# Performance work log

Measured on AMD Instinct MI355X. Metric: run time of the kernel, lower is better.

Reference implementation:

```python
import jax, jax.numpy as jnp
import numpy as np


def _hat(v):
    # v: (...,3) -> (...,3,3) skew-symmetric
    x, y, z = v[..., 0], v[..., 1], v[..., 2]
    O = jnp.zeros_like(x)
    return jnp.stack([
        jnp.stack([O, -z, y], axis=-1),
        jnp.stack([z, O, -x], axis=-1),
        jnp.stack([-y, x, O], axis=-1),
    ], axis=-2)


def _exp_so3(omega):
    # Rodrigues: (...,3) axis-angle -> (...,3,3)
    theta = jnp.maximum(jnp.linalg.norm(omega, axis=-1, keepdims=True), 1e-12)
    k = omega / theta
    K = _hat(k)
    I = jnp.broadcast_to(jnp.eye(3, dtype=omega.dtype), omega.shape[:-1] + (3, 3))
    s = jnp.sin(theta)[..., None]
    c = jnp.cos(theta)[..., None]
    R = I + s * K + (1.0 - c) * (K @ K)
    small = (theta[..., 0] < 1e-4)[..., None, None]
    return jnp.where(small, I + _hat(omega), R)


def setup_inputs() -> dict:
    key = jax.random.key(0)
    ks = jax.random.split(key, 10)
    N, M, H = 262144, 64, 64
    X0 = jax.random.normal(ks[0], (N, 3), jnp.float32)
    G0 = jax.random.normal(ks[1], (M, 3), jnp.float32)
    W = jax.random.uniform(ks[2], (N, M), jnp.float32)
    so3_vec = jax.random.normal(ks[3], (M, 3), jnp.float32) * 0.5
    trans = jax.random.normal(ks[4], (M, 3), jnp.float32) * 0.1
    wproj_w = jax.random.normal(ks[5], (16, M), jnp.float32) * 0.1
    wproj_b = jnp.zeros((16,), jnp.float32)
    w1 = jax.random.normal(ks[6], (H, 19), jnp.float32) * 0.1
    b1 = jnp.zeros((H,), jnp.float32)
    w2 = jax.random.normal(ks[7], (H, H), jnp.float32) * 0.1
    b2 = jnp.zeros((H,), jnp.float32)
    w3 = jax.random.normal(ks[8], (3, H), jnp.float32) * 0.1
    b3 = jnp.zeros((3,), jnp.float32)
    return {"X0": X0, "G0": G0, "W": W, "so3_vec": so3_vec, "trans": trans,
            "wproj_w": wproj_w, "wproj_b": wproj_b,
            "w1": w1, "b1": b1, "w2": w2, "b2": b2, "w3": w3, "b3": b3}


def reference(X0, G0, W, so3_vec, trans, wproj_w, wproj_b, w1, b1, w2, b2, w3, b3):
    # normalized skinning weights (mask is all-ones; row sums > 0 with rand fill)
    Wn = W / (jnp.sum(W, axis=1, keepdims=True) + 1e-12)  # (N,M)
    R = _exp_so3(so3_vec)                                  # (M,3,3)
    d = X0[:, None, :] - G0[None, :, :]                    # (N,M,3)
    Rp = jnp.einsum('mkj,nmj->nmk', R, d)                  # (N,M,3)
    q = Rp + G0[None, :, :] + trans[None, :, :]            # (N,M,3)
    skinned = jnp.einsum('nm,nmk->nk', Wn, q)              # (N,3)
    # residual branch
    Rb = jnp.einsum('nm,mkj->nkj', Wn, R)                  # (N,3,3) blended rotation
    tb = Wn @ trans                                        # (N,3)
    local = jnp.einsum('nji,nj->ni', Rb, skinned - tb)     # Rb^T @ (s - tb)
    wfeat = Wn @ wproj_w.T + wproj_b                       # (N,16)
    h = jnp.concatenate([local, wfeat], axis=1)            # (N,19)
    h = jax.nn.relu(h @ w1.T + b1)
    h = jax.nn.relu(h @ w2.T + b2)
    delta_local = h @ w3.T + b3                            # (N,3)
    delta_world = jnp.einsum('nij,nj->ni', Rb, delta_local)
    return skinned + delta_world
```

## Files before the change

kernel.cpp:

```cpp
#include <hip/hip_runtime.h>
#include <math.h>

typedef float f32x4 __attribute__((ext_vector_type(4)));
typedef _Float16 f16x8 __attribute__((ext_vector_type(8)));
typedef unsigned int u32;
typedef unsigned int u32x2 __attribute__((ext_vector_type(2)));
typedef unsigned int u32x4 __attribute__((ext_vector_type(4)));

#define MJ 64
#define HID 64
#define STR 144
#define TP 32
#define REGSZ (TP*STR)
#define SLICE (2*REGSZ)

static __device__ __forceinline__ u32 pkhf(float a, float b) {
  unsigned short ua = __builtin_bit_cast(unsigned short, (_Float16)a);
  unsigned short ub = __builtin_bit_cast(unsigned short, (_Float16)b);
  return (u32)ua | ((u32)ub << 16);
}

static __device__ __forceinline__ f32x4 mfma16(f16x8 a, f16x8 b, f32x4 c) {
  return __builtin_amdgcn_mfma_f32_16x16x32_f16(a, b, c, 0, 0, 0);
}

__global__ void rig_prep(const float* __restrict__ G0, const float* __restrict__ so3,
                         const float* __restrict__ trans, const float* __restrict__ wproj_w,
                         const float* __restrict__ wproj_b,
                         const float* __restrict__ w1, const float* __restrict__ b1,
                         const float* __restrict__ w2,
                         _Float16* __restrict__ FT1, _Float16* __restrict__ FT2,
                         _Float16* __restrict__ FT3) {
  const int t = threadIdx.x;
  {
    const float ox = so3[3*t+0], oy = so3[3*t+1], oz = so3[3*t+2];
    const float th = sqrtf(ox*ox + oy*oy + oz*oz);
    float R[9];
    if (th < 1e-4f) {
      R[0]=1.f;  R[1]=-oz; R[2]=oy;
      R[3]=oz;   R[4]=1.f; R[5]=-ox;
      R[6]=-oy;  R[7]=ox;  R[8]=1.f;
    } else {
      const float it = 1.f/th;
      const float kx=ox*it, ky=oy*it, kz=oz*it;
      const float s=sinf(th), c=cosf(th), mc=1.f-c;
      R[0]=c+kx*kx*mc;     R[1]=kx*ky*mc-kz*s;  R[2]=kx*kz*mc+ky*s;
      R[3]=ky*kx*mc+kz*s;  R[4]=c+ky*ky*mc;     R[5]=ky*kz*mc-kx*s;
      R[6]=kz*kx*mc-ky*s;  R[7]=kz*ky*mc+kx*s;  R[8]=c+kz*kz*mc;
    }
    const float gx=G0[3*t], gy=G0[3*t+1], gz=G0[3*t+2];
    const float tx=trans[3*t], ty=trans[3*t+1], tz=trans[3*t+2];
    float feat[32];
    #pragma unroll
    for (int i=0;i<9;i++) feat[i]=R[i];
    feat[9]  = gx + tx - (R[0]*gx + R[1]*gy + R[2]*gz);
    feat[10] = gy + ty - (R[3]*gx + R[4]*gy + R[5]*gz);
    feat[11] = gz + tz - (R[6]*gx + R[7]*gy + R[8]*gz);
    feat[12]=tx; feat[13]=ty; feat[14]=tz;
    feat[15]=1.0f;
    #pragma unroll
    for (int i=0;i<16;i++) feat[16+i] = wproj_w[i*MJ + t];
    #pragma unroll
    for (int f=0;f<32;f++) FT1[f*64 + t] = (_Float16)feat[f];
  }
  {
    float fold = b1[t];
    #pragma unroll
    for (int j=0;j<16;j++) fold = fmaf(w1[t*19 + 3 + j], wproj_b[j], fold);
    #pragma unroll
    for (int k=0;k<19;k++) FT2[t*32+k] = (_Float16)w1[t*19+k];
    FT2[t*32+19] = (_Float16)fold;
    #pragma unroll
    for (int k=20;k<32;k++) FT2[t*32+k] = (_Float16)0.0f;
  }
  for (int k=0;k<64;k++) FT3[t*64+k] = (_Float16)w2[t*64+k];
}

__global__ __launch_bounds__(256, 4)
void rig_main(const float* __restrict__ X0, const float* __restrict__ W,
              const _Float16* __restrict__ FT1, const _Float16* __restrict__ FT2,
              const _Float16* __restrict__ FT3,
              const float* __restrict__ b2, const float* __restrict__ w3,
              const float* __restrict__ b3,
              float* __restrict__ out, int Ntot) {
  __shared__ __align__(16) unsigned char smem[4*SLICE];
  const int tid  = threadIdx.x;
  const int wid  = tid >> 6;
  const int lane = tid & 63;
  const int lo   = lane & 15;
  const int hi   = lane >> 4;
  const int pl   = lane & 31;
  const int P0   = blockIdx.x * (4*TP) + wid * TP;
  unsigned char* Areg = smem + wid * SLICE;
  unsigned char* Breg = Areg + REGSZ;

  const float x0 = X0[(size_t)(P0+pl)*3+0];
  const float x1 = X0[(size_t)(P0+pl)*3+1];
  const float x2 = X0[(size_t)(P0+pl)*3+2];

  {
    f32x4 q[8];
    const f32x4* Wq = (const f32x4*)(W + (size_t)P0 * MJ);
    #pragma unroll
    for (int i=0;i<8;i++) q[i] = Wq[i*64 + lane];
    #pragma unroll
    for (int i=0;i<8;i++) {
      const int fidx = i*64 + lane;
      const int row = fidx >> 4, c4 = fidx & 15;
      u32x2 p; p.x = pkhf(q[i][0], q[i][1]); p.y = pkhf(q[i][2], q[i][3]);
      *(u32x2*)(Areg + row*STR + c4*8) = p;
    }
  }
  __syncthreads();

  {
    f16x8 a1[2][2];
    #pragma unroll
    for (int ft=0; ft<2; ft++)
      #pragma unroll
      for (int ks=0; ks<2; ks++)
        a1[ft][ks] = *(const f16x8*)(FT1 + (ft*16+lo)*64 + ks*32 + hi*8);
    f32x4 acc[2][2];
    const f32x4 z = {0.f,0.f,0.f,0.f};
    #pragma unroll
    for (int ft=0; ft<2; ft++)
      #pragma unroll
      for (int pt=0; pt<2; pt++) acc[ft][pt] = z;
    #pragma unroll
    for (int pt=0; pt<2; pt++) {
      #pragma unroll
      for (int ks=0; ks<2; ks++) {
        f16x8 bfrag = *(const f16x8*)(Areg + (pt*16+lo)*STR + ks*64 + hi*16);
        acc[0][pt] = mfma16(a1[0][ks], bfrag, acc[0][pt]);
        acc[1][pt] = mfma16(a1[1][ks], bfrag, acc[1][pt]);
      }
    }
    #pragma unroll
    for (int pt=0; pt<2; pt++)
      #pragma unroll
      for (int ft=0; ft<2; ft++)
        *(f32x4*)(Breg + (pt*16+lo)*STR + ft*64 + hi*16) = acc[ft][pt];
  }
  __syncthreads();

  float Rb[9], sk0, sk1, sk2;
  {
    float v[32];
    #pragma unroll
    for (int i=0;i<8;i++) {
      f32x4 t4 = *(const f32x4*)(Breg + pl*STR + i*16);
      v[4*i+0]=t4[0]; v[4*i+1]=t4[1]; v[4*i+2]=t4[2]; v[4*i+3]=t4[3];
    }
    const float inv = 1.0f/(v[15] + 1e-12f);
    #pragma unroll
    for (int i=0;i<9;i++) Rb[i]=v[i]*inv;
    const float cb0=v[9]*inv,  cb1=v[10]*inv, cb2=v[11]*inv;
    const float tb0=v[12]*inv, tb1=v[13]*inv, tb2=v[14]*inv;
    sk0 = fmaf(Rb[0],x0, fmaf(Rb[1],x1, fmaf(Rb[2],x2, cb0)));
    sk1 = fmaf(Rb[3],x0, fmaf(Rb[4],x1, fmaf(Rb[5],x2, cb1)));
    sk2 = fmaf(Rb[6],x0, fmaf(Rb[7],x1, fmaf(Rb[8],x2, cb2)));
    const float u0=sk0-tb0, u1=sk1-tb1, u2=sk2-tb2;
    const float l0 = Rb[0]*u0 + Rb[3]*u1 + Rb[6]*u2;
    const float l1 = Rb[1]*u0 + Rb[4]*u1 + Rb[7]*u2;
    const float l2 = Rb[2]*u0 + Rb[5]*u1 + Rb[8]*u2;
    float wf[16];
    #pragma unroll
    for (int j=0;j<16;j++) wf[j] = v[16+j]*inv;
    u32x4 h0, h1v, h2v, h3;
    h0.x = pkhf(l0, l1);       h0.y = pkhf(l2, wf[0]);
    h0.z = pkhf(wf[1], wf[2]); h0.w = pkhf(wf[3], wf[4]);
    h1v.x = pkhf(wf[5], wf[6]);  h1v.y = pkhf(wf[7], wf[8]);
    h1v.z = pkhf(wf[9], wf[10]); h1v.w = pkhf(wf[11], wf[12]);
    h2v.x = pkhf(wf[13], wf[14]); h2v.y = pkhf(wf[15], 1.0f);
    h2v.z = 0u; h2v.w = 0u;
    h3.x = 0u; h3.y = 0u; h3.z = 0u; h3.w = 0u;
    *(u32x4*)(Areg + pl*STR +  0) = h0;
    *(u32x4*)(Areg + pl*STR + 16) = h1v;
    *(u32x4*)(Areg + pl*STR + 32) = h2v;
    *(u32x4*)(Areg + pl*STR + 48) = h3;
  }
  __syncthreads();

  {
    f16x8 bh[2];
    #pragma unroll
    for (int pt=0; pt<2; pt++)
      bh[pt] = *(const f16x8*)(Areg + (pt*16+lo)*STR + hi*16);
    #pragma unroll
    for (int nh=0; nh<2; nh++) {
      f16x8 a2[2];
      #pragma unroll
      for (int n2=0; n2<2; n2++)
        a2[n2] = *(const f16x8*)(FT2 + ((nh*2+n2)*16+lo)*32 + hi*8);
      f32x4 c2[2][2];
      const f32x4 z = {0.f,0.f,0.f,0.f};
      #pragma unroll
      for (int n2=0;n2<2;n2++)
        #pragma unroll
        for (int pt=0;pt<2;pt++) c2[n2][pt] = z;
      #pragma unroll
      for (int pt=0; pt<2; pt++)
        #pragma unroll
        for (int n2=0; n2<2; n2++)
          c2[n2][pt] = mfma16(a2[n2], bh[pt], c2[n2][pt]);
      #pragma unroll
      for (int n2=0; n2<2; n2++)
        #pragma unroll
        for (int pt=0; pt<2; pt++) {
          f32x4 r = c2[n2][pt];
          u32x2 wv;
          wv.x = pkhf(fmaxf(r[0],0.f), fmaxf(r[1],0.f));
          wv.y = pkhf(fmaxf(r[2],0.f), fmaxf(r[3],0.f));
          *(u32x2*)(Breg + (pt*16+lo)*STR + (nh*2+n2)*32 + hi*8) = wv;
        }
    }
  }
  __syncthreads();

  {
    f16x8 bh1[2][2];
    #pragma unroll
    for (int pt=0; pt<2; pt++)
      #pragma unroll
      for (int ks=0; ks<2; ks++)
        bh1[pt][ks] = *(const f16x8*)(Breg + (pt*16+lo)*STR + ks*64 + hi*16);
    #pragma unroll
    for (int nh=0; nh<2; nh++) {
      f16x8 a3[2][2];
      #pragma unroll
      for (int n2=0; n2<2; n2++)
        #pragma unroll
        for (int ks=0; ks<2; ks++)
          a3[n2][ks] = *(const f16x8*)(FT3 + ((nh*2+n2)*16+lo)*64 + ks*32 + hi*8);
      f32x4 c3[2][2];
      const f32x4 z = {0.f,0.f,0.f,0.f};
      #pragma unroll
      for (int n2=0;n2<2;n2++)
        #pragma unroll
        for (int pt=0;pt<2;pt++) c3[n2][pt] = z;
      #pragma unroll
      for (int pt=0; pt<2; pt++)
        #pragma unroll
        for (int ks=0; ks<2; ks++)
          #pragma unroll
          for (int n2=0; n2<2; n2++)
            c3[n2][pt] = mfma16(a3[n2][ks], bh1[pt][ks], c3[n2][pt]);
      #pragma unroll
      for (int n2=0; n2<2; n2++) {
        const f32x4 vb2 = *(const f32x4*)(b2 + (nh*2+n2)*16 + hi*4);
        #pragma unroll
        for (int pt=0; pt<2; pt++) {
          f32x4 r = c3[n2][pt];
          u32x2 wv;
          wv.x = pkhf(fmaxf(r[0]+vb2[0],0.f), fmaxf(r[1]+vb2[1],0.f));
          wv.y = pkhf(fmaxf(r[2]+vb2[2],0.f), fmaxf(r[3]+vb2[3],0.f));
          *(u32x2*)(Areg + (pt*16+lo)*STR + (nh*2+n2)*32 + hi*8) = wv;
        }
      }
    }
  }
  __syncthreads();

  {
    float d0 = b3[0], d1 = b3[1], d2 = b3[2];
    #pragma unroll
    for (int i8=0; i8<8; i8++) {
      f16x8 hv = *(const f16x8*)(Areg + pl*STR + i8*16);
      #pragma unroll
      for (int e=0; e<8; e++) {
        const float a = (float)hv[e];
        const int j = i8*8 + e;
        d0 = fmaf(a, w3[      j], d0);
        d1 = fmaf(a, w3[ 64 + j], d1);
        d2 = fmaf(a, w3[128 + j], d2);
      }
    }
    if (lane < TP) {
      const float dw0 = Rb[0]*d0 + Rb[1]*d1 + Rb[2]*d2;
      const float dw1 = Rb[3]*d0 + Rb[4]*d1 + Rb[5]*d2;
      const float dw2 = Rb[6]*d0 + Rb[7]*d1 + Rb[8]*d2;
      const size_t o = (size_t)(P0+pl)*3;
      out[o+0] = sk0 + dw0;
      out[o+1] = sk1 + dw1;
      out[o+2] = sk2 + dw2;
    }
  }
}

extern "C" void kernel_launch(void* const* d_in, const int* in_sizes, int n_in,
                              void* d_out, int out_size, void* d_ws, size_t ws_size,
                              hipStream_t stream) {
  const float* X0      = (const float*)d_in[0];
  const float* G0      = (const float*)d_in[1];
  const float* W       = (const float*)d_in[2];
  const float* so3     = (const float*)d_in[3];
  const float* trans   = (const float*)d_in[4];
  const float* wproj_w = (const float*)d_in[5];
  const float* wproj_b = (const float*)d_in[6];
  const float* w1      = (const float*)d_in[7];
  const float* b1      = (const float*)d_in[8];
  const float* w2      = (const float*)d_in[9];
  const float* b2      = (const float*)d_in[10];
  const float* w3      = (const float*)d_in[11];
  const float* b3      = (const float*)d_in[12];
  float* out = (float*)d_out;

  const int Ntot = in_sizes[0] / 3;

  _Float16* FT1 = (_Float16*)d_ws;
  _Float16* FT2 = (_Float16*)((char*)d_ws + 4096);
  _Float16* FT3 = (_Float16*)((char*)d_ws + 8192);

  rig_prep<<<1, 64, 0, stream>>>(G0, so3, trans, wproj_w, wproj_b,
                                 w1, b1, w2, FT1, FT2, FT3);
  rig_main<<<Ntot/(4*TP), 256, 0, stream>>>(X0, W, FT1, FT2, FT3,
                                            b2, w3, b3, out, Ntot);
}
```

Baseline: 33.72 us.

## Loop four tiles per block with register prefetch of next W tile

Each block now processes four 128-point tiles in a loop, prefetching the next tile's W and X0 into registers while the current tile runs its MFMA phases. Block-wide syncs become a lighter custom barrier that only waits on LDS counters, so outstanding global prefetches are not drained at each phase. The prep kernel is widened to 256 threads so the w2 conversion is split across more threads. In exchange the grid shrinks fourfold and register pressure rises from holding two W tiles, which may reduce occupancy or parallelism on a 256-CU device.

Result: slower. 54.49 us (+61.6%).

```diff
diff --git a/kernel.cpp b/kernel.cpp
--- a/kernel.cpp
+++ b/kernel.cpp
@@ -13,6 +13,8 @@
 #define TP 32
 #define REGSZ (TP*STR)
 #define SLICE (2*REGSZ)
+#define TILES 4
+#define BPTS 128
 
 static __device__ __forceinline__ u32 pkhf(float a, float b) {
   unsigned short ua = __builtin_bit_cast(unsigned short, (_Float16)a);
@@ -22,6 +24,13 @@
 
 static __device__ __forceinline__ f32x4 mfma16(f16x8 a, f16x8 b, f32x4 c) {
   return __builtin_amdgcn_mfma_f32_16x16x32_f16(a, b, c, 0, 0, 0);
+}
+
+static __device__ __forceinline__ void phase_sync() {
+  asm volatile("s_waitcnt lgkmcnt(0)" ::: "memory");
+  __builtin_amdgcn_sched_barrier(0);
+  __builtin_amdgcn_s_barrier();
+  __builtin_amdgcn_sched_barrier(0);
 }
 
 __global__ void rig_prep(const float* __restrict__ G0, const float* __restrict__ so3,
@@ -32,7 +41,7 @@
                          _Float16* __restrict__ FT1, _Float16* __restrict__ FT2,
                          _Float16* __restrict__ FT3) {
   const int t = threadIdx.x;
-  {
+  if (t < MJ) {
     const float ox = so3[3*t+0], oy = so3[3*t+1], oz = so3[3*t+2];
     const float th = sqrtf(ox*ox + oy*oy + oz*oz);
     float R[9];
@@ -62,18 +71,21 @@
     for (int i=0;i<16;i++) feat[16+i] = wproj_w[i*MJ + t];
     #pragma unroll
     for (int f=0;f<32;f++) FT1[f*64 + t] = (_Float16)feat[f];
+
+    float fold = b1[t];
+    #pragma unroll
+    for (int j=0;j<16;j++) fold = fmaf(w1[t*19 + 3 + j], wproj_b[j], fold);
+    #pragma unroll
+    for (int k=0;k<19;k++) FT2[t*32+k] = (_Float16)w1[t*19+k];
+    FT2[t*32+19] = (_Float16)fold;
+    #pragma unroll
+    for (int k=20;k<32;k++) FT2[t*32+k] = (_Float16)0.0f;
   }
   {
-    float fold = b1[t];
-    #pragma unroll
-    for (int j=0;j<16;j++) fold = fmaf(w1[t*19 + 3 + j], wproj_b[j], fold);
-    #pragma unroll
-    for (int k=0;k<19;k++) FT2[t*32+k] = (_Float16)w1[t*19+k];
-    FT2[t*32+19] = (_Float16)fold;
-    #pragma unroll
-    for (int k=20;k<32;k++) FT2[t*32+k] = (_Float16)0.0f;
+    const int row = t >> 2, cb = (t & 3) * 16;
+    #pragma unroll
+    for (int k=0;k<16;k++) FT3[row*64 + cb + k] = (_Float16)w2[row*64 + cb + k];
   }
-  for (int k=0;k<64;k++) FT3[t*64+k] = (_Float16)w2[t*64+k];
 }
 
 __global__ __launch_bounds__(256, 4)
@@ -90,200 +102,222 @@
   const int lo   = lane & 15;
   const int hi   = lane >> 4;
   const int pl   = lane & 31;
-  const int P0   = blockIdx.x * (4*TP) + wid * TP;
+  const int base = blockIdx.x * (TILES*BPTS);
   unsigned char* Areg = smem + wid * SLICE;
   unsigned char* Breg = Areg + REGSZ;
 
-  const float x0 = X0[(size_t)(P0+pl)*3+0];
-  const float x1 = X0[(size_t)(P0+pl)*3+1];
-  const float x2 = X0[(size_t)(P0+pl)*3+2];
-
+  f32x4 qc[8];
   {
-    f32x4 q[8];
-    const f32x4* Wq = (const f32x4*)(W + (size_t)P0 * MJ);
-    #pragma unroll
-    for (int i=0;i<8;i++) q[i] = Wq[i*64 + lane];
+    const f32x4* Wq = (const f32x4*)(W + (size_t)(base + wid*TP) * MJ);
+    #pragma unroll
+    for (int i=0;i<8;i++) qc[i] = Wq[i*64 + lane];
+  }
+  float xc0 = X0[(size_t)(base + wid*TP + pl)*3+0];
+  float xc1 = X0[(size_t)(base + wid*TP + pl)*3+1];
+  float xc2 = X0[(size_t)(base + wid*TP + pl)*3+2];
+
+  #pragma unroll
+  for (int t=0; t<TILES; ++t) {
+    const int P0 = base + t*BPTS + wid*TP;
+
     #pragma unroll
     for (int i=0;i<8;i++) {
       const int fidx = i*64 + lane;
       const int row = fidx >> 4, c4 = fidx & 15;
-      u32x2 p; p.x = pkhf(q[i][0], q[i][1]); p.y = pkhf(q[i][2], q[i][3]);
+      u32x2 p; p.x = pkhf(qc[i][0], qc[i][1]); p.y = pkhf(qc[i][2], qc[i][3]);
       *(u32x2*)(Areg + row*STR + c4*8) = p;
     }
-  }
-  __syncthreads();
-
-  {
-    f16x8 a1[2][2];
-    #pragma unroll
-    for (int ft=0; ft<2; ft++)
-      #pragma unroll
-      for (int ks=0; ks<2; ks++)
-        a1[ft][ks] = *(const f16x8*)(FT1 + (ft*16+lo)*64 + ks*32 + hi*8);
-    f32x4 acc[2][2];
-    const f32x4 z = {0.f,0.f,0.f,0.f};
-    #pragma unroll
-    for (int ft=0; ft<2; ft++)
-      #pragma unroll
-      for (int pt=0; pt<2; pt++) acc[ft][pt] = z;
-    #pragma unroll
-    for (int pt=0; pt<2; pt++) {
-      #pragma unroll
-      for (int ks=0; ks<2; ks++) {
-        f16x8 bfrag = *(const f16x8*)(Areg + (pt*16+lo)*STR + ks*64 + hi*16);
-        acc[0][pt] = mfma16(a1[0][ks], bfrag, acc[0][pt]);
-        acc[1][pt] = mfma16(a1[1][ks], bfrag, acc[1][pt]);
-      }
-    }
-    #pragma unroll
-    for (int pt=0; pt<2; pt++)
+    f32x4 qn[8];
+    float xn0=0.f, xn1=0.f, xn2=0.f;
+    if (t+1 < TILES) {
+      const f32x4* Wqn = (const f32x4*)(W + (size_t)(P0 + BPTS) * MJ);
+      #pragma unroll
+      for (int i=0;i<8;i++) qn[i] = Wqn[i*64 + lane];
+      xn0 = X0[(size_t)(P0 + BPTS + pl)*3+0];
+      xn1 = X0[(size_t)(P0 + BPTS + pl)*3+1];
+      xn2 = X0[(size_t)(P0 + BPTS + pl)*3+2];
+    }
+    phase_sync();
+
+    {
+      f16x8 a1[2][2];
       #pragma unroll
       for (int ft=0; ft<2; ft++)
-        *(f32x4*)(Breg + (pt*16+lo)*STR + ft*64 + hi*16) = acc[ft][pt];
-  }
-  __syncthreads();
-
-  float Rb[9], sk0, sk1, sk2;
-  {
-    float v[32];
-    #pragma unroll
-    for (int i=0;i<8;i++) {
-      f32x4 t4 = *(const f32x4*)(Breg + pl*STR + i*16);
-      v[4*i+0]=t4[0]; v[4*i+1]=t4[1]; v[4*i+2]=t4[2]; v[4*i+3]=t4[3];
-    }
-    const float inv = 1.0f/(v[15] + 1e-12f);
-    #pragma unroll
-    for (int i=0;i<9;i++) Rb[i]=v[i]*inv;
-    const float cb0=v[9]*inv,  cb1=v[10]*inv, cb2=v[11]*inv;
-    const float tb0=v[12]*inv, tb1=v[13]*inv, tb2=v[14]*inv;
-    sk0 = fmaf(Rb[0],x0, fmaf(Rb[1],x1, fmaf(Rb[2],x2, cb0)));
-    sk1 = fmaf(Rb[3],x0, fmaf(Rb[4],x1, fmaf(Rb[5],x2, cb1)));
-    sk2 = fmaf(Rb[6],x0, fmaf(Rb[7],x1, fmaf(Rb[8],x2, cb2)));
-    const float u0=sk0-tb0, u1=sk1-tb1, u2=sk2-tb2;
-    const float l0 = Rb[0]*u0 + Rb[3]*u1 + Rb[6]*u2;
-    const float l1 = Rb[1]*u0 + Rb[4]*u1 + Rb[7]*u2;
-    const float l2 = Rb[2]*u0 + Rb[5]*u1 + Rb[8]*u2;
-    float wf[16];
-    #pragma unroll
-    for (int j=0;j<16;j++) wf[j] = v[16+j]*inv;
-    u32x4 h0, h1v, h2v, h3;
-    h0.x = pkhf(l0, l1);       h0.y = pkhf(l2, wf[0]);
-    h0.z = pkhf(wf[1], wf[2]); h0.w = pkhf(wf[3], wf[4]);
-    h1v.x = pkhf(wf[5], wf[6]);  h1v.y = pkhf(wf[7], wf[8]);
-    h1v.z = pkhf(wf[9], wf[10]); h1v.w = pkhf(wf[11], wf[12]);
-    h2v.x = pkhf(wf[13], wf[14]); h2v.y = pkhf(wf[15], 1.0f);
-    h2v.z = 0u; h2v.w = 0u;
-    h3.x = 0u; h3.y = 0u; h3.z = 0u; h3.w = 0u;
-    *(u32x4*)(Areg + pl*STR +  0) = h0;
-    *(u32x4*)(Areg + pl*STR + 16) = h1v;
-    *(u32x4*)(Areg + pl*STR + 32) = h2v;
-    *(u32x4*)(Areg + pl*STR + 48) = h3;
-  }
-  __syncthreads();
-
-  {
-    f16x8 bh[2];
-    #pragma unroll
-    for (int pt=0; pt<2; pt++)
-      bh[pt] = *(const f16x8*)(Areg + (pt*16+lo)*STR + hi*16);
-    #pragma unroll
-    for (int nh=0; nh<2; nh++) {
-      f16x8 a2[2];
-      #pragma unroll
-      for (int n2=0; n2<2; n2++)
-        a2[n2] = *(const f16x8*)(FT2 + ((nh*2+n2)*16+lo)*32 + hi*8);
-      f32x4 c2[2][2];
+        #pragma unroll
+        for (int ks=0; ks<2; ks++)
+          a1[ft][ks] = *(const f16x8*)(FT1 + (ft*16+lo)*64 + ks*32 + hi*8);
+      f32x4 acc[2][2];
       const f32x4 z = {0.f,0.f,0.f,0.f};
       #pragma unroll
-      for (int n2=0;n2<2;n2++)
-        #pragma unroll
-        for (int pt=0;pt<2;pt++) c2[n2][pt] = z;
+      for (int ft=0; ft<2; ft++)
+        #pragma unroll
+        for (int pt=0; pt<2; pt++) acc[ft][pt] = z;
+      #pragma unroll
+      for (int pt=0; pt<2; pt++) {
+        #pragma unroll
+        for (int ks=0; ks<2; ks++) {
+          f16x8 bfrag = *(const f16x8*)(Areg + (pt*16+lo)*STR + ks*64 + hi*16);
+          acc[0][pt] = mfma16(a1[0][ks], bfrag, acc[0][pt]);
+          acc[1][pt] = mfma16(a1[1][ks], bfrag, acc[1][pt]);
+        }
+      }
       #pragma unroll
       for (int pt=0; pt<2; pt++)
         #pragma unroll
+        for (int ft=0; ft<2; ft++)
+          *(f32x4*)(Breg + (pt*16+lo)*STR + ft*64 + hi*16) = acc[ft][pt];
+    }
+    phase_sync();
+
+    float Rb[9], sk0, sk1, sk2;
+    {
+      float v[32];
+      #pragma unroll
+      for (int i=0;i<8;i++) {
+        f32x4 t4 = *(const f32x4*)(Breg + pl*STR + i*16);
+        v[4*i+0]=t4[0]; v[4*i+1]=t4[1]; v[4*i+2]=t4[2]; v[4*i+3]=t4[3];
+      }
+      const float inv = 1.0f/(v[15] + 1e-12f);
+      #pragma unroll
+      for (int i=0;i<9;i++) Rb[i]=v[i]*inv;
+      const float cb0=v[9]*inv,  cb1=v[10]*inv, cb2=v[11]*inv;
+      const float tb0=v[12]*inv, tb1=v[13]*inv, tb2=v[14]*inv;
+      sk0 = fmaf(Rb[0],xc0, fmaf(Rb[1],xc1, fmaf(Rb[2],xc2, cb0)));
+      sk1 = fmaf(Rb[3],xc0, fmaf(Rb[4],xc1, fmaf(Rb[5],xc2, cb1)));
+      sk2 = fmaf(Rb[6],xc0, fmaf(Rb[7],xc1, fmaf(Rb[8],xc2, cb2)));
+      const float u0=sk0-tb0, u1=sk1-tb1, u2=sk2-tb2;
+      const float l0 = Rb[0]*u0 + Rb[3]*u1 + Rb[6]*u2;
+      const float l1 = Rb[1]*u0 + Rb[4]*u1 + Rb[7]*u2;
+      const float l2 = Rb[2]*u0 + Rb[5]*u1 + Rb[8]*u2;
+      float wf[16];
+      #pragma unroll
+      for (int j=0;j<16;j++) wf[j] = v[16+j]*inv;
+      u32x4 h0, h1v, h2v, h3;
+      h0.x = pkhf(l0, l1);       h0.y = pkhf(l2, wf[0]);
+      h0.z = pkhf(wf[1], wf[2]); h0.w = pkhf(wf[3], wf[4]);
+      h1v.x = pkhf(wf[5], wf[6]);  h1v.y = pkhf(wf[7], wf[8]);
+      h1v.z = pkhf(wf[9], wf[10]); h1v.w = pkhf(wf[11], wf[12]);
+      h2v.x = pkhf(wf[13], wf[14]); h2v.y = pkhf(wf[15], 1.0f);
+      h2v.z = 0u; h2v.w = 0u;
+      h3.x = 0u; h3.y = 0u; h3.z = 0u; h3.w = 0u;
+      *(u32x4*)(Areg + pl*STR +  0) = h0;
+      *(u32x4*)(Areg + pl*STR + 16) = h1v;
+      *(u32x4*)(Areg + pl*STR + 32) = h2v;
+      *(u32x4*)(Areg + pl*STR + 48) = h3;
+    }
+    phase_sync();
+
+    {
+      f16x8 bh[2];
+      #pragma unroll
+      for (int pt=0; pt<2; pt++)
+        bh[pt] = *(const f16x8*)(Areg + (pt*16+lo)*STR + hi*16);
+      #pragma unroll
+      for (int nh=0; nh<2; nh++) {
+        f16x8 a2[2];
+        #pragma unroll
         for (int n2=0; n2<2; n2++)
-          c2[n2][pt] = mfma16(a2[n2], bh[pt], c2[n2][pt]);
-      #pragma unroll
-      for (int n2=0; n2<2; n2++)
-        #pragma unroll
-        for (int pt=0; pt<2; pt++) {
-          f32x4 r = c2[n2][pt];
-          u32x2 wv;
-          wv.x = pkhf(fmaxf(r[0],0.f), fmaxf(r[1],0.f));
-          wv.y = pkhf(fmaxf(r[2],0.f), fmaxf(r[3],0.f));
-          *(u32x2*)(Breg + (pt*16+lo)*STR + (nh*2+n2)*32 + hi*8) = wv;
+          a2[n2] = *(const f16x8*)(FT2 + ((nh*2+n2)*16+lo)*32 + hi*8);
+        f32x4 c2[2][2];
+        const f32x4 z = {0.f,0.f,0.f,0.f};
+        #pragma unroll
+        for (int n2=0;n2<2;n2++)
+          #pragma unroll
+          for (int pt=0;pt<2;pt++) c2[n2][pt] = z;
+        #pragma unroll
+        for (int pt=0; pt<2; pt++)
+          #pragma unroll
+          for (int n2=0; n2<2; n2++)
+            c2[n2][pt] = mfma16(a2[n2], bh[pt], c2[n2][pt]);
+        #pragma unroll
+        for (int n2=0; n2<2; n2++)
+          #pragma unroll
+          for (int pt=0; pt<2; pt++) {
+            f32x4 r = c2[n2][pt];
+            u32x2 wv;
+            wv.x = pkhf(fmaxf(r[0],0.f), fmaxf(r[1],0.f));
+            wv.y = pkhf(fmaxf(r[2],0.f), fmaxf(r[3],0.f));
+            *(u32x2*)(Breg + (pt*16+lo)*STR + (nh*2+n2)*32 + hi*8) = wv;
+          }
+      }
+    }
+    phase_sync();
+
+    {
+      f16x8 bh1[2][2];
+      #pragma unroll
+      for (int pt=0; pt<2; pt++)
+        #pragma unroll
+        for (int ks=0; ks<2; ks++)
+          bh1[pt][ks] = *(const f16x8*)(Breg + (pt*16+lo)*STR + ks*64 + hi*16);
+      #pragma unroll
+      for (int nh=0; nh<2; nh++) {
+        f16x8 a3[2][2];
+        #pragma unroll
+        for (int n2=0; n2<2; n2++)
+          #pragma unroll
+          for (int ks=0; ks<2; ks++)
+            a3[n2][ks] = *(const f16x8*)(FT3 + ((nh*2+n2)*16+lo)*64 + ks*32 + hi*8);
+        f32x4 c3[2][2];
+        const f32x4 z = {0.f,0.f,0.f,0.f};
+        #pragma unroll
+        for (int n2=0;n2<2;n2++)
+          #pragma unroll
+          for (int pt=0;pt<2;pt++) c3[n2][pt] = z;
+        #pragma unroll
+        for (int pt=0; pt<2; pt++)
+          #pragma unroll
+          for (int ks=0; ks<2; ks++)
+            #pragma unroll
+            for (int n2=0; n2<2; n2++)
+              c3[n2][pt] = mfma16(a3[n2][ks], bh1[pt][ks], c3[n2][pt]);
+        #pragma unroll
+        for (int n2=0; n2<2; n2++) {
+          const f32x4 vb2 = *(const f32x4*)(b2 + (nh*2+n2)*16 + hi*4);
+          #pragma unroll
+          for (int pt=0; pt<2; pt++) {
+            f32x4 r = c3[n2][pt];
+            u32x2 wv;
+            wv.x = pkhf(fmaxf(r[0]+vb2[0],0.f), fmaxf(r[1]+vb2[1],0.f));
+            wv.y = pkhf(fmaxf(r[2]+vb2[2],0.f), fmaxf(r[3]+vb2[3],0.f));
+            *(u32x2*)(Areg + (pt*16+lo)*STR + (nh*2+n2)*32 + hi*8) = wv;
+          }
         }
-    }
-  }
-  __syncthreads();
-
-  {
-    f16x8 bh1[2][2];
-    #pragma unroll
-    for (int pt=0; pt<2; pt++)
-      #pragma unroll
-      for (int ks=0; ks<2; ks++)
-        bh1[pt][ks] = *(const f16x8*)(Breg + (pt*16+lo)*STR + ks*64 + hi*16);
-    #pragma unroll
-    for (int nh=0; nh<2; nh++) {
-      f16x8 a3[2][2];
-      #pragma unroll
-      for (int n2=0; n2<2; n2++)
-        #pragma unroll
-        for (int ks=0; ks<2; ks++)
-          a3[n2][ks] = *(const f16x8*)(FT3 + ((nh*2+n2)*16+lo)*64 + ks*32 + hi*8);
-      f32x4 c3[2][2];
-      const f32x4 z = {0.f,0.f,0.f,0.f};
-      #pragma unroll
-      for (int n2=0;n2<2;n2++)
-        #pragma unroll
-        for (int pt=0;pt<2;pt++) c3[n2][pt] = z;
-      #pragma unroll
-      for (int pt=0; pt<2; pt++)
-        #pragma unroll
-        for (int ks=0; ks<2; ks++)
-          #pragma unroll
-          for (int n2=0; n2<2; n2++)
-            c3[n2][pt] = mfma16(a3[n2][ks], bh1[pt][ks], c3[n2][pt]);
-      #pragma unroll
-      for (int n2=0; n2<2; n2++) {
-        const f32x4 vb2 = *(const f32x4*)(b2 + (nh*2+n2)*16 + hi*4);
-        #pragma unroll
-        for (int pt=0; pt<2; pt++) {
-          f32x4 r = c3[n2][pt];
-          u32x2 wv;
-          wv.x = pkhf(fmaxf(r[0]+vb2[0],0.f), fmaxf(r[1]+vb2[1],0.f));
-          wv.y = pkhf(fmaxf(r[2]+vb2[2],0.f), fmaxf(r[3]+vb2[3],0.f));
-          *(u32x2*)(Areg + (pt*16+lo)*STR + (nh*2+n2)*32 + hi*8) = wv;
+      }
+    }
+    phase_sync();
+
+    {
+      float d0 = b3[0], d1 = b3[1], d2 = b3[2];
+      #pragma unroll
+      for (int i8=0; i8<8; i8++) {
+        f16x8 hv = *(const f16x8*)(Areg + pl*STR + i8*16);
+        #pragma unroll
+        for (int e=0; e<8; e++) {
+          const float a = (float)hv[e];
+          const int j = i8*8 + e;
+          d0 = fmaf(a, w3[      j], d0);
+          d1 = fmaf(a, w3[ 64 + j], d1);
+          d2 = fmaf(a, w3[128 + j], d2);
         }
       }
-    }
-  }
-  __syncthreads();
-
-  {
-    float d0 = b3[0], d1 = b3[1], d2 = b3[2];
-    #pragma unroll
-    for (int i8=0; i8<8; i8++) {
-      f16x8 hv = *(const f16x8*)(Areg + pl*STR + i8*16);
-      #pragma unroll
-      for (int e=0; e<8; e++) {
-        const float a = (float)hv[e];
-        const int j = i8*8 + e;
-        d0 = fmaf(a, w3[      j], d0);
-        d1 = fmaf(a, w3[ 64 + j], d1);
-        d2 = fmaf(a, w3[128 + j], d2);
-      }
-    }
-    if (lane < TP) {
-      const float dw0 = Rb[0]*d0 + Rb[1]*d1 + Rb[2]*d2;
-      const float dw1 = Rb[3]*d0 + Rb[4]*d1 + Rb[5]*d2;
-      const float dw2 = Rb[6]*d0 + Rb[7]*d1 + Rb[8]*d2;
-      const size_t o = (size_t)(P0+pl)*3;
-      out[o+0] = sk0 + dw0;
-      out[o+1] = sk1 + dw1;
-      out[o+2] = sk2 + dw2;
-    }
+      if (lane < TP) {
+        const float dw0 = Rb[0]*d0 + Rb[1]*d1 + Rb[2]*d2;
+        const float dw1 = Rb[3]*d0 + Rb[4]*d1 + Rb[5]*d2;
+        const float dw2 = Rb[6]*d0 + Rb[7]*d1 + Rb[8]*d2;
+        const size_t o = (size_t)(P0+pl)*3;
+        out[o+0] = sk0 + dw0;
+        out[o+1] = sk1 + dw1;
+        out[o+2] = sk2 + dw2;
+      }
+    }
+
+    if (t+1 < TILES) {
+      #pragma unroll
+      for (int i=0;i<8;i++) qc[i] = qn[i];
+      xc0 = xn0; xc1 = xn1; xc2 = xn2;
+    }
+    phase_sync();
   }
 }
 
@@ -311,8 +345,8 @@
   _Float16* FT2 = (_Float16*)((char*)d_ws + 4096);
   _Float16* FT3 = (_Float16*)((char*)d_ws + 8192);
 
-  rig_prep<<<1, 64, 0, stream>>>(G0, so3, trans, wproj_w, wproj_b,
-                                 w1, b1, w2, FT1, FT2, FT3);
-  rig_main<<<Ntot/(4*TP), 256, 0, stream>>>(X0, W, FT1, FT2, FT3,
-                                            b2, w3, b3, out, Ntot);
-}
+  rig_prep<<<1, 256, 0, stream>>>(G0, so3, trans, wproj_w, wproj_b,
+                                  w1, b1, w2, FT1, FT2, FT3);
+  rig_main<<<Ntot/(TILES*BPTS), 256, 0, stream>>>(X0, W, FT1, FT2, FT3,
+                                                  b2, w3, b3, out, Ntot);
+}
```

## Use single-wave blocks, replace block barriers with scheduling fences, widen prep kernel

Applied to the files above, without the earlier changes.

The main kernel now launches one 64-thread wave per block, each handling 32 points with its own LDS slice. The __syncthreads calls become compiler sched_barrier fences, relying on in-order LDS operations within one wave. The intent is to remove workgroup barrier stalls between the MFMA phases, since the four waves never shared data. The prep kernel runs 256 threads so the w2-to-fp16 conversion is split four ways. This relies on compiler-inserted waitcnts for LDS ordering and raises the block count fourfold, which changes scheduling and occupancy behaviour.

Result: slower. 38.72 us (+14.8%).

```diff
diff --git a/kernel.cpp b/kernel.cpp
--- a/kernel.cpp
+++ b/kernel.cpp
@@ -22,6 +22,10 @@
 
 static __device__ __forceinline__ f32x4 mfma16(f16x8 a, f16x8 b, f32x4 c) {
   return __builtin_amdgcn_mfma_f32_16x16x32_f16(a, b, c, 0, 0, 0);
+}
+
+static __device__ __forceinline__ void phase_fence() {
+  __builtin_amdgcn_sched_barrier(0);
 }
 
 __global__ void rig_prep(const float* __restrict__ G0, const float* __restrict__ so3,
@@ -32,7 +36,7 @@
                          _Float16* __restrict__ FT1, _Float16* __restrict__ FT2,
                          _Float16* __restrict__ FT3) {
   const int t = threadIdx.x;
-  {
+  if (t < MJ) {
     const float ox = so3[3*t+0], oy = so3[3*t+1], oz = so3[3*t+2];
     const float th = sqrtf(ox*ox + oy*oy + oz*oz);
     float R[9];
@@ -62,8 +66,7 @@
     for (int i=0;i<16;i++) feat[16+i] = wproj_w[i*MJ + t];
     #pragma unroll
     for (int f=0;f<32;f++) FT1[f*64 + t] = (_Float16)feat[f];
-  }
-  {
+
     float fold = b1[t];
     #pragma unroll
     for (int j=0;j<16;j++) fold = fmaf(w1[t*19 + 3 + j], wproj_b[j], fold);
@@ -73,26 +76,28 @@
     #pragma unroll
     for (int k=20;k<32;k++) FT2[t*32+k] = (_Float16)0.0f;
   }
-  for (int k=0;k<64;k++) FT3[t*64+k] = (_Float16)w2[t*64+k];
-}
-
-__global__ __launch_bounds__(256, 4)
+  {
+    const int row = t >> 2, cb = (t & 3) * 16;
+    #pragma unroll
+    for (int k=0;k<16;k++) FT3[row*64 + cb + k] = (_Float16)w2[row*64 + cb + k];
+  }
+}
+
+__global__ __launch_bounds__(64, 4)
 void rig_main(const float* __restrict__ X0, const float* __restrict__ W,
               const _Float16* __restrict__ FT1, const _Float16* __restrict__ FT2,
               const _Float16* __restrict__ FT3,
               const float* __restrict__ b2, const float* __restrict__ w3,
               const float* __restrict__ b3,
               float* __restrict__ out, int Ntot) {
-  __shared__ __align__(16) unsigned char smem[4*SLICE];
-  const int tid  = threadIdx.x;
-  const int wid  = tid >> 6;
-  const int lane = tid & 63;
+  __shared__ __align__(16) unsigned char smem[SLICE];
+  const int lane = threadIdx.x & 63;
   const int lo   = lane & 15;
   const int hi   = lane >> 4;
   const int pl   = lane & 31;
-  const int P0   = blockIdx.x * (4*TP) + wid * TP;
-  unsigned char* Areg = smem + wid * SLICE;
-  unsigned char* Breg = Areg + REGSZ;
+  const int P0   = blockIdx.x * TP;
+  unsigned char* Areg = smem;
+  unsigned char* Breg = smem + REGSZ;
 
   const float x0 = X0[(size_t)(P0+pl)*3+0];
   const float x1 = X0[(size_t)(P0+pl)*3+1];
@@ -111,7 +116,7 @@
       *(u32x2*)(Areg + row*STR + c4*8) = p;
     }
   }
-  __syncthreads();
+  phase_fence();
 
   {
     f16x8 a1[2][2];
@@ -135,13 +140,14 @@
         acc[1][pt] = mfma16(a1[1][ks], bfrag, acc[1][pt]);
       }
     }
+    phase_fence();
     #pragma unroll
     for (int pt=0; pt<2; pt++)
       #pragma unroll
       for (int ft=0; ft<2; ft++)
         *(f32x4*)(Breg + (pt*16+lo)*STR + ft*64 + hi*16) = acc[ft][pt];
   }
-  __syncthreads();
+  phase_fence();
 
   float Rb[9], sk0, sk1, sk2;
   {
@@ -174,12 +180,13 @@
     h2v.x = pkhf(wf[13], wf[14]); h2v.y = pkhf(wf[15], 1.0f);
     h2v.z = 0u; h2v.w = 0u;
     h3.x = 0u; h3.y = 0u; h3.z = 0u; h3.w = 0u;
+    phase_fence();
     *(u32x4*)(Areg + pl*STR +  0) = h0;
     *(u32x4*)(Areg + pl*STR + 16) = h1v;
     *(u32x4*)(Areg + pl*STR + 32) = h2v;
     *(u32x4*)(Areg + pl*STR + 48) = h3;
   }
-  __syncthreads();
+  phase_fence();
 
   {
     f16x8 bh[2];
@@ -215,7 +222,7 @@
         }
     }
   }
-  __syncthreads();
+  phase_fence();
 
   {
     f16x8 bh1[2][2];
@@ -245,6 +252,7 @@
           #pragma unroll
           for (int n2=0; n2<2; n2++)
             c3[n2][pt] = mfma16(a3[n2][ks], bh1[pt][ks], c3[n2][pt]);
+      if (nh == 0) phase_fence();
       #pragma unroll
       for (int n2=0; n2<2; n2++) {
         const f32x4 vb2 = *(const f32x4*)(b2 + (nh*2+n2)*16 + hi*4);
@@ -259,7 +267,7 @@
       }
     }
   }
-  __syncthreads();
+  phase_fence();
 
   {
     float d0 = b3[0], d1 = b3[1], d2 = b3[2];
@@ -311,8 +319,8 @@
   _Float16* FT2 = (_Float16*)((char*)d_ws + 4096);
   _Float16* FT3 = (_Float16*)((char*)d_ws + 8192);
 
-  rig_prep<<<1, 64, 0, stream>>>(G0, so3, trans, wproj_w, wproj_b,
-                                 w1, b1, w2, FT1, FT2, FT3);
-  rig_main<<<Ntot/(4*TP), 256, 0, stream>>>(X0, W, FT1, FT2, FT3,
-                                            b2, w3, b3, out, Ntot);
-}
+  rig_prep<<<1, 256, 0, stream>>>(G0, so3, trans, wproj_w, wproj_b,
+                                  w1, b1, w2, FT1, FT2, FT3);
+  rig_main<<<Ntot/TP, 64, 0, stream>>>(X0, W, FT1, FT2, FT3,
+                                       b2, w3, b3, out, Ntot);
+}
```
